# Kernel tuning notes

Hardware: AMD Instinct MI355X
Metric: run time of the kernel (lower is better)

## Reference

```python
import jax, jax.numpy as jnp
import numpy as np

N = 50000      # nodes
E = 800000     # edges (avg degree 16)
IN_DIM = 256
OUT_DIM = 64
HEADS = 4
P_L = 0.1      # freq='low' slope


def setup_inputs() -> dict:
    key = jax.random.key(0)
    ks = jax.random.split(key, 12)
    h = jax.random.normal(ks[0], (N, IN_DIM), dtype=jnp.float32)
    src = jax.random.randint(ks[1], (E,), 0, N, dtype=jnp.int32)
    dst = jax.random.randint(ks[2], (E,), 0, N, dtype=jnp.int32)
    d = jax.random.uniform(ks[3], (N,), dtype=jnp.float32)  # degree norm per node
    s_in = 1.0 / np.sqrt(IN_DIM)
    s_d = 1.0 / np.sqrt(OUT_DIM)
    W_in = jax.random.normal(ks[4], (IN_DIM, HEADS * OUT_DIM), dtype=jnp.float32) * s_in
    b_in = jnp.zeros((HEADS * OUT_DIM,), dtype=jnp.float32)
    W_att = jax.random.normal(ks[5], (HEADS, OUT_DIM, OUT_DIM), dtype=jnp.float32) * s_d
    b_att = jnp.zeros((HEADS, OUT_DIM), dtype=jnp.float32)
    W_g = jax.random.normal(ks[6], (HEADS, 2 * OUT_DIM), dtype=jnp.float32) * s_d
    b_g = jnp.zeros((HEADS,), dtype=jnp.float32)
    W_out = jax.random.normal(ks[7], (HEADS * OUT_DIM, OUT_DIM), dtype=jnp.float32) * s_d
    b_out = jnp.zeros((OUT_DIM,), dtype=jnp.float32)
    return {"h": h, "src": src, "dst": dst, "d": d,
            "W_in": W_in, "b_in": b_in, "W_att": W_att, "b_att": b_att,
            "W_g": W_g, "b_g": b_g, "W_out": W_out, "b_out": b_out}


def reference(h, src, dst, d, W_in, b_in, W_att, b_att, W_g, b_g, W_out, b_out):
    # node transform: [N, H, D]  (dropout is identity in eval mode)
    hh = jax.nn.relu(h @ W_in + b_in).reshape(-1, HEADS, OUT_DIM)
    # per-head att_gate applied at node level (same math as per-edge, cheaper)
    a = jnp.einsum('nhd,hde->nhe', hh, W_att) + b_att           # [N, H, D]
    # gate linear on concat([dst_a, src_a]) split into the two halves of W_g
    g_dst = jnp.einsum('nhd,hd->nh', a, W_g[:, :OUT_DIM])        # [N, H]
    g_src = jnp.einsum('nhd,hd->nh', a, W_g[:, OUT_DIM:])        # [N, H]
    _h = g_dst[dst] + g_src[src] + b_g                           # [E, H]
    # freq='low': relu(where(_h>0, _h, -p_l*_h)) == where(_h>0, _h, -p_l*_h)
    g = jnp.where(_h > 0, _h, -P_L * _h)
    alpha = g * (d[dst] * d[src])[:, None]                       # [E, H]
    msg = hh[src] * alpha[..., None]                             # [E, H, D]
    z = jax.ops.segment_sum(msg, dst, num_segments=N)            # [N, H, D]
    return z.reshape(-1, HEADS * OUT_DIM) @ W_out + b_out        # [N, D]
```

## Files before the change

kernel.cpp:

```cpp
#include <hip/hip_runtime.h>
#include <hip/hip_bf16.h>

#define N_NODES 50000
#define N_EDGES 800000
#define IN_DIM 256
#define OUT_DIM 64
#define HEADS 4
#define HD 256
#define P_L 0.1f
#define TILE_N 64
#define CAP 64
#define OVCAP 4096

typedef __attribute__((ext_vector_type(8))) short bf16x8;
typedef __attribute__((ext_vector_type(4))) float f32x4;

static __device__ __forceinline__ short f2bf(float f) {
    __hip_bfloat16 b = __float2bfloat16(f);
    return *(short*)&b;
}

__global__ __launch_bounds__(256) void precompute_kernel(
    const float* __restrict__ W_att, const float* __restrict__ b_att,
    const float* __restrict__ W_g,
    float* __restrict__ v_dst, float* __restrict__ v_src,
    float* __restrict__ c_dst, float* __restrict__ c_src) {
    int t = threadIdx.x;
    int h = t >> 6, dd = t & 63;
    float sd = 0.f, ss = 0.f;
    for (int e = 0; e < 64; ++e) {
        float w = W_att[h * 4096 + dd * 64 + e];
        sd += w * W_g[h * 128 + e];
        ss += w * W_g[h * 128 + 64 + e];
    }
    v_dst[t] = sd;
    v_src[t] = ss;
    if (dd == 0) {
        float cd = 0.f, cs = 0.f;
        for (int e = 0; e < 64; ++e) {
            float b = b_att[h * 64 + e];
            cd += b * W_g[h * 128 + e];
            cs += b * W_g[h * 128 + 64 + e];
        }
        c_dst[h] = cd;
        c_src[h] = cs;
    }
}

__global__ __launch_bounds__(256) void wconv_kernel(
    const float* __restrict__ W_in, const float* __restrict__ W_out,
    short* __restrict__ W_bt, short* __restrict__ W_obt2) {
    int b = blockIdx.x, t = threadIdx.x;
    if (b < 256) {
        W_bt[t * 256 + b] = f2bf(W_in[b * 256 + t]);
    } else {
        int flat = (b - 256) * 256 + t;
        int k = flat & 63, oc = (flat >> 6) & 63, h = flat >> 12;
        W_obt2[flat] = f2bf(W_out[(h * 64 + k) * 64 + oc]);
    }
}

__global__ __launch_bounds__(256, 2) void node_mfma_kernel(
    const float* __restrict__ hin, const short* __restrict__ W_bt,
    const short* __restrict__ W_obt2, const float* __restrict__ b_in,
    const float* __restrict__ v_dst, const float* __restrict__ v_src,
    const float* __restrict__ c_dst, const float* __restrict__ c_src,
    __hip_bfloat16* __restrict__ y, float* __restrict__ gd,
    float* __restrict__ gs) {
    __shared__ short A_lds[TILE_N * 256];
    int t = threadIdx.x;
    int n0 = blockIdx.x * TILE_N;
    bool full = (n0 + TILE_N) <= N_NODES;

    #pragma unroll
    for (int rr = 0; rr < 4; ++rr) {
        int r = rr * 16 + (t >> 4), c0 = (t & 15) * 16;
        int row = n0 + r;
        if (row > N_NODES - 1) row = N_NODES - 1;
        const float* hp = hin + (size_t)row * IN_DIM + c0;
        float fv[16];
        *(float4*)&fv[0]  = *(const float4*)(hp + 0);
        *(float4*)&fv[4]  = *(const float4*)(hp + 4);
        *(float4*)&fv[8]  = *(const float4*)(hp + 8);
        *(float4*)&fv[12] = *(const float4*)(hp + 12);
        short sv[16];
        #pragma unroll
        for (int j = 0; j < 16; ++j) sv[j] = f2bf(fv[j]);
        int swz = (r & 7) << 3;
        int base = r * 256 + c0;
        *(bf16x8*)&A_lds[(base + 0) ^ swz] = *(bf16x8*)&sv[0];
        *(bf16x8*)&A_lds[(base + 8) ^ swz] = *(bf16x8*)&sv[8];
    }
    __syncthreads();

    int l = t & 63, w = t >> 6;
    int lr = l & 15, lg = l >> 4;
    int aswz = (lr & 7) << 3;

    f32x4 acc[4][4];
    #pragma unroll
    for (int rt = 0; rt < 4; ++rt)
        #pragma unroll
        for (int ct = 0; ct < 4; ++ct) acc[rt][ct] = (f32x4){0.f, 0.f, 0.f, 0.f};

    #pragma unroll
    for (int ks = 0; ks < 8; ++ks) {
        bf16x8 bfrag[4], afrag[4];
        #pragma unroll
        for (int ct = 0; ct < 4; ++ct)
            bfrag[ct] = *(const bf16x8*)(W_bt + (size_t)(w * 64 + ct * 16 + lr) * 256 + ks * 32 + lg * 8);
        #pragma unroll
        for (int rt = 0; rt < 4; ++rt)
            afrag[rt] = *(bf16x8*)&A_lds[((rt * 16 + lr) * 256 + ks * 32 + lg * 8) ^ aswz];
        #pragma unroll
        for (int rt = 0; rt < 4; ++rt)
            #pragma unroll
            for (int ct = 0; ct < 4; ++ct)
                acc[rt][ct] = __builtin_amdgcn_mfma_f32_16x16x32_bf16(afrag[rt], bfrag[ct], acc[rt][ct], 0, 0, 0);
    }

    int col[4];
    float vd[4], vs[4], bi[4];
    #pragma unroll
    for (int ct = 0; ct < 4; ++ct) {
        col[ct] = w * 64 + ct * 16 + lr;
        bi[ct] = b_in[col[ct]];
        vd[ct] = v_dst[col[ct]];
        vs[ct] = v_src[col[ct]];
    }
    float pd[4][4], ps[4][4];
    #pragma unroll
    for (int rt = 0; rt < 4; ++rt)
        #pragma unroll
        for (int r = 0; r < 4; ++r) { pd[rt][r] = 0.f; ps[rt][r] = 0.f; }
    #pragma unroll
    for (int rt = 0; rt < 4; ++rt)
        #pragma unroll
        for (int ct = 0; ct < 4; ++ct)
            #pragma unroll
            for (int r = 0; r < 4; ++r) {
                float v = fmaxf(acc[rt][ct][r] + bi[ct], 0.f);
                acc[rt][ct][r] = v;
                pd[rt][r] += v * vd[ct];
                ps[rt][r] += v * vs[ct];
            }
    #pragma unroll
    for (int rt = 0; rt < 4; ++rt)
        #pragma unroll
        for (int r = 0; r < 4; ++r) {
            #pragma unroll
            for (int off = 1; off < 16; off <<= 1) {
                pd[rt][r] += __shfl_xor(pd[rt][r], off, 64);
                ps[rt][r] += __shfl_xor(ps[rt][r], off, 64);
            }
        }
    if (lr == 0) {
        float cd = c_dst[w], cs = c_src[w];
        #pragma unroll
        for (int rt = 0; rt < 4; ++rt)
            #pragma unroll
            for (int r = 0; r < 4; ++r) {
                int m = rt * 16 + lg * 4 + r;
                if (full || (n0 + m) < N_NODES) {
                    gd[(n0 + m) * HEADS + w] = pd[rt][r] + cd;
                    gs[(n0 + m) * HEADS + w] = ps[rt][r] + cs;
                }
            }
    }

    __syncthreads();
    #pragma unroll
    for (int rt = 0; rt < 4; ++rt)
        #pragma unroll
        for (int ct = 0; ct < 4; ++ct)
            #pragma unroll
            for (int r = 0; r < 4; ++r) {
                int m = rt * 16 + lg * 4 + r;
                int idx = m * 256 + col[ct];
                A_lds[idx ^ (((lg * 4 + r) & 7) << 3)] = f2bf(acc[rt][ct][r]);
            }
    __syncthreads();

    f32x4 acc2[4][4];
    #pragma unroll
    for (int rt = 0; rt < 4; ++rt)
        #pragma unroll
        for (int ct = 0; ct < 4; ++ct) acc2[rt][ct] = (f32x4){0.f, 0.f, 0.f, 0.f};
    #pragma unroll
    for (int ks = 0; ks < 2; ++ks) {
        bf16x8 bfrag[4], afrag[4];
        #pragma unroll
        for (int ct = 0; ct < 4; ++ct)
            bfrag[ct] = *(const bf16x8*)(W_obt2 + (size_t)(w * 64 + ct * 16 + lr) * 64 + ks * 32 + lg * 8);
        #pragma unroll
        for (int rt = 0; rt < 4; ++rt)
            afrag[rt] = *(bf16x8*)&A_lds[((rt * 16 + lr) * 256 + w * 64 + ks * 32 + lg * 8) ^ aswz];
        #pragma unroll
        for (int rt = 0; rt < 4; ++rt)
            #pragma unroll
            for (int ct = 0; ct < 4; ++ct)
                acc2[rt][ct] = __builtin_amdgcn_mfma_f32_16x16x32_bf16(afrag[rt], bfrag[ct], acc2[rt][ct], 0, 0, 0);
    }
    #pragma unroll
    for (int rt = 0; rt < 4; ++rt)
        #pragma unroll
        for (int ct = 0; ct < 4; ++ct)
            #pragma unroll
            for (int r = 0; r < 4; ++r) {
                int m = rt * 16 + lg * 4 + r;
                if (full || (n0 + m) < N_NODES)
                    y[(size_t)(n0 + m) * HD + w * 64 + ct * 16 + lr] =
                        __float2bfloat16(acc2[rt][ct][r]);
            }
}

__global__ __launch_bounds__(256) void fill_kernel(
    const int* __restrict__ src, const int* __restrict__ dst,
    int* __restrict__ cursor, int* __restrict__ bucket_src,
    int* __restrict__ ov_list, int* __restrict__ ov_count) {
    int e = blockIdx.x * 256 + threadIdx.x;
    if (e >= N_EDGES) return;
    int n = dst[e];
    int pos = atomicAdd(&cursor[n], 1);
    if (pos < CAP) {
        bucket_src[(size_t)n * CAP + pos] = src[e];
    } else {
        int oi = atomicAdd(ov_count, 1);
        if (oi < OVCAP) ov_list[oi] = e;
    }
}

__global__ __launch_bounds__(256) void agg_kernel(
    const int* __restrict__ bucket_src, const int* __restrict__ cursor,
    const int* __restrict__ src, const int* __restrict__ dst,
    const int* __restrict__ ov_list, const int* __restrict__ ov_count,
    const float* __restrict__ dnorm, const float* __restrict__ b_g,
    const __hip_bfloat16* __restrict__ y, const float* __restrict__ gd,
    const float* __restrict__ gs, const float* __restrict__ b_out,
    float* __restrict__ out) {
    int t = threadIdx.x;
    int wv = t >> 6, lane = t & 63;
    int half = lane >> 5, sl = lane & 31;
    int n = blockIdx.x * 8 + wv * 2 + half;
    int head = sl >> 3;
    int deg = cursor[n];
    if (deg > CAP) deg = CAP;
    float dn = dnorm[n];
    float gdh = gd[n * HEADS + head] + b_g[head];
    int degmax = max(deg, __shfl_xor(deg, 32, 64));

    const uint4* yb = (const uint4*)y;
    const int* bp = bucket_src + (size_t)n * CAP;
    float a[8];
    #pragma unroll
    for (int j = 0; j < 8; ++j) a[j] = 0.f;

    for (int i = 0; i < degmax; i += 8) {
        int sarr[8];
        #pragma unroll
        for (int j = 0; j < 8; ++j) {
            int e = i + j;
            sarr[j] = (e < deg) ? bp[e] : -1;
        }
        float gsv[8], dnv[8];
        uint4 v[8];
        #pragma unroll
        for (int j = 0; j < 8; ++j) {
            int s = sarr[j] < 0 ? 0 : sarr[j];
            gsv[j] = gs[s * HEADS + head];
            dnv[j] = dnorm[s];
            v[j] = yb[(size_t)s * 32 + sl];
        }
        #pragma unroll
        for (int j = 0; j < 8; ++j) {
            float _h = gdh + gsv[j];
            float g = _h > 0.f ? _h : -P_L * _h;
            float al = (sarr[j] < 0) ? 0.f : g * dn * dnv[j];
            a[0] += __uint_as_float(v[j].x << 16) * al;
            a[1] += __uint_as_float(v[j].x & 0xffff0000u) * al;
            a[2] += __uint_as_float(v[j].y << 16) * al;
            a[3] += __uint_as_float(v[j].y & 0xffff0000u) * al;
            a[4] += __uint_as_float(v[j].z << 16) * al;
            a[5] += __uint_as_float(v[j].z & 0xffff0000u) * al;
            a[6] += __uint_as_float(v[j].w << 16) * al;
            a[7] += __uint_as_float(v[j].w & 0xffff0000u) * al;
        }
    }

    int cnt = *ov_count;
    if (cnt > 0) {
        if (cnt > OVCAP) cnt = OVCAP;
        for (int j = 0; j < cnt; ++j) {
            int e = ov_list[j];
            if (dst[e] == n) {
                int s = src[e];
                float _h = gdh + gs[s * HEADS + head];
                float g = _h > 0.f ? _h : -P_L * _h;
                float al = g * dn * dnorm[s];
                uint4 vv = yb[(size_t)s * 32 + sl];
                a[0] += __uint_as_float(vv.x << 16) * al;
                a[1] += __uint_as_float(vv.x & 0xffff0000u) * al;
                a[2] += __uint_as_float(vv.y << 16) * al;
                a[3] += __uint_as_float(vv.y & 0xffff0000u) * al;
                a[4] += __uint_as_float(vv.z << 16) * al;
                a[5] += __uint_as_float(vv.z & 0xffff0000u) * al;
                a[6] += __uint_as_float(vv.w << 16) * al;
                a[7] += __uint_as_float(vv.w & 0xffff0000u) * al;
            }
        }
    }

    #pragma unroll
    for (int j = 0; j < 8; ++j) {
        a[j] += __shfl_xor(a[j], 8, 64);
        a[j] += __shfl_xor(a[j], 16, 64);
    }
    if (sl < 8) {
        float4 b0 = *(const float4*)&b_out[sl * 8];
        float4 b1 = *(const float4*)&b_out[sl * 8 + 4];
        float4 o0, o1;
        o0.x = a[0] + b0.x; o0.y = a[1] + b0.y; o0.z = a[2] + b0.z; o0.w = a[3] + b0.w;
        o1.x = a[4] + b1.x; o1.y = a[5] + b1.y; o1.z = a[6] + b1.z; o1.w = a[7] + b1.w;
        *(float4*)&out[(size_t)n * OUT_DIM + sl * 8] = o0;
        *(float4*)&out[(size_t)n * OUT_DIM + sl * 8 + 4] = o1;
    }
}

extern "C" void kernel_launch(void* const* d_in, const int* in_sizes, int n_in,
                              void* d_out, int out_size, void* d_ws, size_t ws_size,
                              hipStream_t stream) {
    const float* h     = (const float*)d_in[0];
    const int*   src   = (const int*)d_in[1];
    const int*   dst   = (const int*)d_in[2];
    const float* dnorm = (const float*)d_in[3];
    const float* W_in  = (const float*)d_in[4];
    const float* b_in  = (const float*)d_in[5];
    const float* W_att = (const float*)d_in[6];
    const float* b_att = (const float*)d_in[7];
    const float* W_g   = (const float*)d_in[8];
    const float* b_g   = (const float*)d_in[9];
    const float* W_out = (const float*)d_in[10];
    const float* b_out = (const float*)d_in[11];
    float* out = (float*)d_out;

    char* ws = (char*)d_ws;
    __hip_bfloat16* y = (__hip_bfloat16*)ws;
    ws += (size_t)N_NODES * HD * sizeof(__hip_bfloat16);
    float* gd    = (float*)ws;  ws += (size_t)N_NODES * HEADS * sizeof(float);
    float* gs    = (float*)ws;  ws += (size_t)N_NODES * HEADS * sizeof(float);
    float* v_dst = (float*)ws;  ws += 256 * sizeof(float);
    float* v_src = (float*)ws;  ws += 256 * sizeof(float);
    float* c_dst = (float*)ws;  ws += 16;
    float* c_src = (float*)ws;  ws += 16;
    int* cursor     = (int*)ws; ws += (size_t)N_NODES * sizeof(int);
    int* ov_count   = (int*)ws; ws += 16;
    int* ov_list    = (int*)ws; ws += OVCAP * sizeof(int);
    int* bucket_src = (int*)ws; ws += (size_t)N_NODES * CAP * sizeof(int);
    short* W_bt     = (short*)ws; ws += 256 * 256 * sizeof(short);
    short* W_obt2   = (short*)ws;

    hipMemsetAsync(cursor, 0, (size_t)N_NODES * sizeof(int), stream);
    hipMemsetAsync(ov_count, 0, sizeof(int), stream);

    precompute_kernel<<<1, 256, 0, stream>>>(W_att, b_att, W_g, v_dst, v_src, c_dst, c_src);
    wconv_kernel<<<320, 256, 0, stream>>>(W_in, W_out, W_bt, W_obt2);
    fill_kernel<<<(N_EDGES + 255) / 256, 256, 0, stream>>>(src, dst, cursor, bucket_src,
                                                           ov_list, ov_count);
    node_mfma_kernel<<<(N_NODES + TILE_N - 1) / TILE_N, 256, 0, stream>>>(
        h, W_bt, W_obt2, b_in, v_dst, v_src, c_dst, c_src, y, gd, gs);
    agg_kernel<<<N_NODES / 8, 256, 0, stream>>>(bucket_src, cursor, src, dst,
                                                ov_list, ov_count, dnorm, b_g,
                                                y, gd, gs, b_out, out);
}
```

Before: 169.4 us.

## Fuse prep kernels and run edge bucketing alongside node MFMA in one launch

Merges the weight-conversion and attention-precompute kernels into one launch, and folds the edge bucket-fill work into extra blocks of the node MFMA kernel so the atomic scatter runs concurrently with the GEMM. Packs per-source gate value and degree norm into a float2 so the aggregation gather does one load instead of two. It also raises the occupancy hint on the fused kernel. This cuts launch count and lets memory-bound fill overlap compute-bound GEMM, at the cost of a heterogeneous kernel whose LDS allocation also applies to fill blocks and a larger gs buffer.

New measurement: 177.9 us. 5.0% more time.

```diff
diff --git a/kernel.cpp b/kernel.cpp
--- a/kernel.cpp
+++ b/kernel.cpp
@@ -11,6 +11,8 @@
 #define TILE_N 64
 #define CAP 64
 #define OVCAP 4096
+#define NODE_BLOCKS 782
+#define FILL_BLOCKS 3125
 
 typedef __attribute__((ext_vector_type(8))) short bf16x8;
 typedef __attribute__((ext_vector_type(4))) float f32x4;
@@ -20,55 +22,72 @@
     return *(short*)&b;
 }
 
-__global__ __launch_bounds__(256) void precompute_kernel(
+__global__ __launch_bounds__(256) void prep_kernel(
     const float* __restrict__ W_att, const float* __restrict__ b_att,
     const float* __restrict__ W_g,
+    const float* __restrict__ W_in, const float* __restrict__ W_out,
+    short* __restrict__ W_bt, short* __restrict__ W_obt2,
     float* __restrict__ v_dst, float* __restrict__ v_src,
     float* __restrict__ c_dst, float* __restrict__ c_src) {
-    int t = threadIdx.x;
-    int h = t >> 6, dd = t & 63;
-    float sd = 0.f, ss = 0.f;
-    for (int e = 0; e < 64; ++e) {
-        float w = W_att[h * 4096 + dd * 64 + e];
-        sd += w * W_g[h * 128 + e];
-        ss += w * W_g[h * 128 + 64 + e];
-    }
-    v_dst[t] = sd;
-    v_src[t] = ss;
-    if (dd == 0) {
-        float cd = 0.f, cs = 0.f;
-        for (int e = 0; e < 64; ++e) {
-            float b = b_att[h * 64 + e];
-            cd += b * W_g[h * 128 + e];
-            cs += b * W_g[h * 128 + 64 + e];
-        }
-        c_dst[h] = cd;
-        c_src[h] = cs;
-    }
-}
-
-__global__ __launch_bounds__(256) void wconv_kernel(
-    const float* __restrict__ W_in, const float* __restrict__ W_out,
-    short* __restrict__ W_bt, short* __restrict__ W_obt2) {
     int b = blockIdx.x, t = threadIdx.x;
     if (b < 256) {
         W_bt[t * 256 + b] = f2bf(W_in[b * 256 + t]);
-    } else {
+    } else if (b < 320) {
         int flat = (b - 256) * 256 + t;
         int k = flat & 63, oc = (flat >> 6) & 63, h = flat >> 12;
         W_obt2[flat] = f2bf(W_out[(h * 64 + k) * 64 + oc]);
-    }
-}
-
-__global__ __launch_bounds__(256, 2) void node_mfma_kernel(
+    } else {
+        int h = t >> 6, dd = t & 63;
+        float sd = 0.f, ss = 0.f;
+        for (int e = 0; e < 64; ++e) {
+            float w = W_att[h * 4096 + dd * 64 + e];
+            sd += w * W_g[h * 128 + e];
+            ss += w * W_g[h * 128 + 64 + e];
+        }
+        v_dst[t] = sd;
+        v_src[t] = ss;
+        if (dd == 0) {
+            float cd = 0.f, cs = 0.f;
+            for (int e = 0; e < 64; ++e) {
+                float bb = b_att[h * 64 + e];
+                cd += bb * W_g[h * 128 + e];
+                cs += bb * W_g[h * 128 + 64 + e];
+            }
+            c_dst[h] = cd;
+            c_src[h] = cs;
+        }
+    }
+}
+
+__global__ __launch_bounds__(256, 3) void fused_nf_kernel(
     const float* __restrict__ hin, const short* __restrict__ W_bt,
     const short* __restrict__ W_obt2, const float* __restrict__ b_in,
     const float* __restrict__ v_dst, const float* __restrict__ v_src,
     const float* __restrict__ c_dst, const float* __restrict__ c_src,
+    const float* __restrict__ dnorm,
+    const int* __restrict__ src, const int* __restrict__ dst,
+    int* __restrict__ cursor, int* __restrict__ bucket_src,
+    int* __restrict__ ov_list, int* __restrict__ ov_count,
     __hip_bfloat16* __restrict__ y, float* __restrict__ gd,
-    float* __restrict__ gs) {
+    float2* __restrict__ gsp) {
     __shared__ short A_lds[TILE_N * 256];
     int t = threadIdx.x;
+
+    if (blockIdx.x >= NODE_BLOCKS) {
+        int e = (blockIdx.x - NODE_BLOCKS) * 256 + t;
+        if (e < N_EDGES) {
+            int n = dst[e];
+            int pos = atomicAdd(&cursor[n], 1);
+            if (pos < CAP) {
+                bucket_src[(size_t)n * CAP + pos] = src[e];
+            } else {
+                int oi = atomicAdd(ov_count, 1);
+                if (oi < OVCAP) ov_list[oi] = e;
+            }
+        }
+        return;
+    }
+
     int n0 = blockIdx.x * TILE_N;
     bool full = (n0 + TILE_N) <= N_NODES;
 
@@ -163,7 +182,8 @@
                 int m = rt * 16 + lg * 4 + r;
                 if (full || (n0 + m) < N_NODES) {
                     gd[(n0 + m) * HEADS + w] = pd[rt][r] + cd;
-                    gs[(n0 + m) * HEADS + w] = ps[rt][r] + cs;
+                    gsp[(n0 + m) * HEADS + w] =
+                        make_float2(ps[rt][r] + cs, dnorm[n0 + m]);
                 }
             }
     }
@@ -212,22 +232,6 @@
                     y[(size_t)(n0 + m) * HD + w * 64 + ct * 16 + lr] =
                         __float2bfloat16(acc2[rt][ct][r]);
             }
-}
-
-__global__ __launch_bounds__(256) void fill_kernel(
-    const int* __restrict__ src, const int* __restrict__ dst,
-    int* __restrict__ cursor, int* __restrict__ bucket_src,
-    int* __restrict__ ov_list, int* __restrict__ ov_count) {
-    int e = blockIdx.x * 256 + threadIdx.x;
-    if (e >= N_EDGES) return;
-    int n = dst[e];
-    int pos = atomicAdd(&cursor[n], 1);
-    if (pos < CAP) {
-        bucket_src[(size_t)n * CAP + pos] = src[e];
-    } else {
-        int oi = atomicAdd(ov_count, 1);
-        if (oi < OVCAP) ov_list[oi] = e;
-    }
 }
 
 __global__ __launch_bounds__(256) void agg_kernel(
@@ -236,7 +240,7 @@
     const int* __restrict__ ov_list, const int* __restrict__ ov_count,
     const float* __restrict__ dnorm, const float* __restrict__ b_g,
     const __hip_bfloat16* __restrict__ y, const float* __restrict__ gd,
-    const float* __restrict__ gs, const float* __restrict__ b_out,
+    const float2* __restrict__ gsp, const float* __restrict__ b_out,
     float* __restrict__ out) {
     int t = threadIdx.x;
     int wv = t >> 6, lane = t & 63;
@@ -262,20 +266,19 @@
             int e = i + j;
             sarr[j] = (e < deg) ? bp[e] : -1;
         }
-        float gsv[8], dnv[8];
+        float2 gg[8];
         uint4 v[8];
         #pragma unroll
         for (int j = 0; j < 8; ++j) {
             int s = sarr[j] < 0 ? 0 : sarr[j];
-            gsv[j] = gs[s * HEADS + head];
-            dnv[j] = dnorm[s];
+            gg[j] = gsp[s * HEADS + head];
             v[j] = yb[(size_t)s * 32 + sl];
         }
         #pragma unroll
         for (int j = 0; j < 8; ++j) {
-            float _h = gdh + gsv[j];
+            float _h = gdh + gg[j].x;
             float g = _h > 0.f ? _h : -P_L * _h;
-            float al = (sarr[j] < 0) ? 0.f : g * dn * dnv[j];
+            float al = (sarr[j] < 0) ? 0.f : g * dn * gg[j].y;
             a[0] += __uint_as_float(v[j].x << 16) * al;
             a[1] += __uint_as_float(v[j].x & 0xffff0000u) * al;
             a[2] += __uint_as_float(v[j].y << 16) * al;
@@ -294,9 +297,10 @@
             int e = ov_list[j];
             if (dst[e] == n) {
                 int s = src[e];
-                float _h = gdh + gs[s * HEADS + head];
+                float2 gg = gsp[s * HEADS + head];
+                float _h = gdh + gg.x;
                 float g = _h > 0.f ? _h : -P_L * _h;
-                float al = g * dn * dnorm[s];
+                float al = g * dn * gg.y;
                 uint4 vv = yb[(size_t)s * 32 + sl];
                 a[0] += __uint_as_float(vv.x << 16) * al;
                 a[1] += __uint_as_float(vv.x & 0xffff0000u) * al;
@@ -346,29 +350,28 @@
     char* ws = (char*)d_ws;
     __hip_bfloat16* y = (__hip_bfloat16*)ws;
     ws += (size_t)N_NODES * HD * sizeof(__hip_bfloat16);
-    float* gd    = (float*)ws;  ws += (size_t)N_NODES * HEADS * sizeof(float);
-    float* gs    = (float*)ws;  ws += (size_t)N_NODES * HEADS * sizeof(float);
-    float* v_dst = (float*)ws;  ws += 256 * sizeof(float);
-    float* v_src = (float*)ws;  ws += 256 * sizeof(float);
-    float* c_dst = (float*)ws;  ws += 16;
-    float* c_src = (float*)ws;  ws += 16;
-    int* cursor     = (int*)ws; ws += (size_t)N_NODES * sizeof(int);
-    int* ov_count   = (int*)ws; ws += 16;
-    int* ov_list    = (int*)ws; ws += OVCAP * sizeof(int);
-    int* bucket_src = (int*)ws; ws += (size_t)N_NODES * CAP * sizeof(int);
+    float* gd     = (float*)ws;  ws += (size_t)N_NODES * HEADS * sizeof(float);
+    float2* gsp   = (float2*)ws; ws += (size_t)N_NODES * HEADS * sizeof(float2);
+    float* v_dst  = (float*)ws;  ws += 256 * sizeof(float);
+    float* v_src  = (float*)ws;  ws += 256 * sizeof(float);
+    float* c_dst  = (float*)ws;  ws += 16;
+    float* c_src  = (float*)ws;  ws += 16;
+    int* cursor     = (int*)ws;  ws += (size_t)N_NODES * sizeof(int);
+    int* ov_count   = (int*)ws;  ws += 16;
+    int* ov_list    = (int*)ws;  ws += OVCAP * sizeof(int);
+    int* bucket_src = (int*)ws;  ws += (size_t)N_NODES * CAP * sizeof(int);
     short* W_bt     = (short*)ws; ws += 256 * 256 * sizeof(short);
     short* W_obt2   = (short*)ws;
 
     hipMemsetAsync(cursor, 0, (size_t)N_NODES * sizeof(int), stream);
     hipMemsetAsync(ov_count, 0, sizeof(int), stream);
 
-    precompute_kernel<<<1, 256, 0, stream>>>(W_att, b_att, W_g, v_dst, v_src, c_dst, c_src);
-    wconv_kernel<<<320, 256, 0, stream>>>(W_in, W_out, W_bt, W_obt2);
-    fill_kernel<<<(N_EDGES + 255) / 256, 256, 0, stream>>>(src, dst, cursor, bucket_src,
-                                                           ov_list, ov_count);
-    node_mfma_kernel<<<(N_NODES + TILE_N - 1) / TILE_N, 256, 0, stream>>>(
-        h, W_bt, W_obt2, b_in, v_dst, v_src, c_dst, c_src, y, gd, gs);
+    prep_kernel<<<321, 256, 0, stream>>>(W_att, b_att, W_g, W_in, W_out,
+                                         W_bt, W_obt2, v_dst, v_src, c_dst, c_src);
+    fused_nf_kernel<<<NODE_BLOCKS + FILL_BLOCKS, 256, 0, stream>>>(
+        h, W_bt, W_obt2, b_in, v_dst, v_src, c_dst, c_src, dnorm,
+        src, dst, cursor, bucket_src, ov_list, ov_count, y, gd, gsp);
     agg_kernel<<<N_NODES / 8, 256, 0, stream>>>(bucket_src, cursor, src, dst,
                                                 ov_list, ov_count, dnorm, b_g,
-                                                y, gd, gs, b_out, out);
-}
+                                                y, gd, gsp, b_out, out);
+}
```
